# Optimization experiments

Measured on AMD Instinct MI355X. Metric: run time of the kernel, lower is better.

Reference implementation:

```python
import jax, jax.numpy as jnp
import numpy as np

# Problem constants (match init_kwargs)
T = 48            # prediction horizon
B = 1024          # batch size
A_SC = 0.999      # A_matrix[0,0]
B00, B01 = 0.95, -1.05   # B_matrix
SMIN, SMAX = 0.0, 13.5   # charge_min_max
PS_MAX = 5.0             # storage_power_min_max[1]
PG_MIN, PG_MAX = -10.0, 10.0  # grid_power_min_max
EPS_W = 1e4              # slack penalty weight in the objective
N_ITERS = 300            # PDHG iterations (fixed, jit-friendly)
DELTA = 1e-6             # tiny strong-convexity regularizer

# Variable layout in x (per sample): [s_0..s_T | Ps_in | Ps_out | Pl | Pr | eps]
# n = 6T+1. Equalities: dynamics (T rows) + s_0 == s0 (1 row). Inequalities: 12T rows.

def _build_matrices(T):
    n = 6 * T + 1
    off_in = T + 1; off_out = off_in + T; off_pl = off_out + T
    off_pr = off_pl + T; off_eps = off_pr + T
    # Equality block E x = b_eq
    E = np.zeros((T + 1, n), np.float32)
    idx = np.arange(T)
    E[idx, idx + 1] = 1.0          # s_{k+1}
    E[idx, idx] = -A_SC            # -A s_k
    E[idx, off_in + idx] = -B00    # -B00 Ps_in_k
    E[idx, off_out + idx] = -B01   # -B01 Ps_out_k
    E[T, 0] = 1.0                  # s_0 == s0
    I = np.eye(T, dtype=np.float32)
    def blk(*pairs):
        g = np.zeros((T, n), np.float32)
        for off, sgn in pairs:
            g[:, off:off + T] += sgn * I
        return g
    # Inequality block G x <= h, grouped by constraint type (order matches h below)
    G = np.concatenate([
        blk((0, -1.0)),                       # -s_k      <= -SMIN
        blk((0, 1.0)),                        #  s_k      <=  SMAX
        blk((off_in, 1.0)),                   #  Ps_in    <=  PS_MAX
        blk((off_in, -1.0)),                  # -Ps_in    <=  0
        blk((off_out, 1.0)),                  #  Ps_out   <=  PS_MAX
        blk((off_out, -1.0)),                 # -Ps_out   <=  0
        blk((off_pl, -1.0), (off_eps, -1.0)), # -Pl - eps <= -load
        blk((off_pl, 1.0), (off_eps, -1.0)),  #  Pl - eps <=  load
        blk((off_pr, -1.0), (off_eps, -1.0)), # -Pr - eps <= -pv
        blk((off_pr, 1.0), (off_eps, -1.0)),  #  Pr - eps <=  pv
        blk((off_pr, -1.0), (off_pl, 1.0), (off_in, 1.0), (off_out, -1.0)),  # -(grid) <= -PG_MIN
        blk((off_pr, 1.0), (off_pl, -1.0), (off_in, -1.0), (off_out, 1.0)),  #  (grid) <=  PG_MAX
    ], 0)
    K = np.concatenate([E, G], 0)
    knorm = float(np.linalg.norm(K, 2))
    return K, knorm

_K_NP, _KNORM = _build_matrices(T)
_K = jnp.asarray(_K_NP)  # (m, n), shared across the batch


def setup_inputs() -> dict:
    key = jax.random.key(0)
    k1, k2, k3, k4 = jax.random.split(key, 4)
    price = jax.random.uniform(k1, (B, T), jnp.float32) * 0.3 + 0.05  # $/kWh
    load = jax.random.uniform(k2, (B, T), jnp.float32) * 5.0           # kW
    pv = jax.random.uniform(k3, (B, T), jnp.float32) * 5.0             # kW
    s0 = jax.random.uniform(k4, (B, 1), jnp.float32) * 10.0 + 1.0      # kWh, in [SMIN,SMAX]
    return {"price_hat": price, "load_hat": load, "pv_hat": pv, "initial_state": s0}


def _solve(price, load, pv, s0):
    """Batched PDHG (Chambolle-Pock) solver for the per-sample LP.
    min c^T x + (DELTA/2)||x||^2  s.t.  E x = b_eq, G x <= h.
    """
    b = price.shape[0]
    zT = jnp.zeros((b, T), price.dtype)
    on = jnp.ones((b, T), price.dtype)
    # objective: -price*(Pr - Pl - Ps_in + Ps_out) + EPS_W*eps
    c = jnp.concatenate([jnp.zeros((b, T + 1), price.dtype),
                         price, -price, price, -price, EPS_W * on], 1)
    b_eq = jnp.concatenate([zT, s0], 1)  # dynamics rhs = 0, then s_0 = s0
    h = jnp.concatenate([-SMIN * on, SMAX * on, PS_MAX * on, zT, PS_MAX * on, zT,
                         -load, load, -pv, pv, -PG_MIN * on, PG_MAX * on], 1)
    q = jnp.concatenate([b_eq, h], 1)  # (b, m)
    n_eq = T + 1
    tau = 0.95 / _KNORM
    sigma = 0.95 / _KNORM
    n = c.shape[1]; m = q.shape[1]

    def step(carry, _):
        x, y = carry
        xn = (x - tau * (c + y @ _K)) / (1.0 + tau * DELTA)
        yb = y + sigma * ((2.0 * xn - x) @ _K.T) - sigma * q
        # equality duals are free; inequality duals projected to >= 0
        yn = jnp.concatenate([yb[:, :n_eq], jnp.maximum(yb[:, n_eq:], 0.0)], 1)
        return (xn, yn), None

    (x, _), _ = jax.lax.scan(step,
                             (jnp.zeros((b, n), price.dtype), jnp.zeros((b, m), price.dtype)),
                             None, length=N_ITERS)
    off = T + 1
    Ps_in = x[:, off:off + T]
    Ps_out = x[:, off + T:off + 2 * T]
    Pl = x[:, off + 2 * T:off + 3 * T]
    Pr = x[:, off + 3 * T:off + 4 * T]
    eps = x[:, off + 4 * T:off + 5 * T]
    return Ps_in, Ps_out, Pl, Pr, eps


def reference(price_hat, load_hat, pv_hat, initial_state):
    return _solve(price_hat, load_hat, pv_hat, initial_state)
```

## Files before the change

kernel.cpp:

```cpp
#include <hip/hip_runtime.h>
#include <math.h>


#define TT 48
#define N_ITERS 300

typedef float v2 __attribute__((ext_vector_type(2)));

__device__ __forceinline__ v2 vfma(v2 a, v2 b, v2 c) {
    return __builtin_elementwise_fma(a, b, c);
}
__device__ __forceinline__ v2 vmax0(v2 a) {
    return __builtin_elementwise_max(a, (v2)(0.f));
}

__device__ __forceinline__ float shift_up(float v, bool is0) {
    int iv  = __float_as_int(v);
    int s48 = __builtin_amdgcn_readlane(iv, 48);
    int sh  = __builtin_amdgcn_update_dpp(iv, iv, 0x138, 0xF, 0xF, false);
    sh = is0 ? s48 : sh;
    return __int_as_float(sh);
}

__device__ __forceinline__ float shift_dn(float v, bool is48) {
    int iv = __float_as_int(v);
    int s0 = __builtin_amdgcn_readlane(iv, 0);
    int sh = __builtin_amdgcn_update_dpp(iv, iv, 0x130, 0xF, 0xF, false);
    sh = is48 ? s0 : sh;
    return __int_as_float(sh);
}

__global__ __launch_bounds__(64) void pdhg_kernel(
    const float* __restrict__ price,
    const float* __restrict__ loadv,
    const float* __restrict__ pvv,
    const float* __restrict__ s0,
    float* __restrict__ out,
    int B,
    float tau)
{
    const int b = blockIdx.x;
    const int t = threadIdx.x;
    const bool lt  = (t < TT);
    const bool i48 = (t == 48);
    const bool i0  = (t == 0);

    const float A  = 0.999f;
    const float Bi = 0.95f;
    const float Bo = -1.05f;
    const float ts = tau * tau;

    float pr_ = 0.f, ld = 0.f, pv_ = 0.f;
    if (lt) {
        pr_ = price[(size_t)b*TT + t];
        ld  = loadv[(size_t)b*TT + t];
        pv_ = pvv  [(size_t)b*TT + t];
    }
    const float qe   = i48 ? s0[b] : 0.f;
    const float tsqe = ts * qe;

    const v2 tsv   = (v2)(ts);
    const v2 ntsv  = (v2)(-ts);
    const v2 npts  = { -ts, ts };
    const v2 BiBov = { -Bi, -Bo };
    const float tsA  = ts * A;
    const float tsBi = ts * Bi;
    const float tsBo = ts * Bo;
    const v2 tpv   = { tau * pr_, -tau * pr_ };
    const float tep = tau * 1.0e4f;
    const v2 C12   = { 0.f,        ts * 13.5f };
    const v2 C35   = { ts * 5.f,   ts * 5.f   };
    const v2 C79   = { ts * (-ld), ts * (-pv_) };
    const v2 C810  = { ts * ld,    ts * pv_   };
    const v2 C1112 = { ts * 10.f,  ts * 10.f  };

    v2 xIO = (v2)(0.f), xPP = (v2)(0.f), xSE = (v2)(0.f);
    float ye = 0.f, yprev = 0.f;
    v2 G12 = (v2)(0.f), G35 = (v2)(0.f), G46 = (v2)(0.f),
       G79 = (v2)(0.f), G810 = (v2)(0.f), G1112 = (v2)(0.f);

    #pragma unroll 2
    for (int it = 0; it < N_ITERS; ++it) {
        const v2 dv    = G1112 - G1112.yx;
        const v2 ktIO  = vfma((v2)(ye), BiBov, (G35 - G46) + dv);
        const v2 ktPP  = (G810 - G79) + dv;
        const v2 S     = G79 + G810;
        const float wep = tep - (S.x + S.y);
        float kts = fmaf(-A, ye, yprev + (G12.y - G12.x));
        kts = lt ? kts : yprev;

        const v2 wIO = ktIO + tpv;
        const v2 wPP = ktPP + tpv;
        const v2 wSE = { kts, wep };
        const v2 xnIO = xIO - wIO;  const v2 zIO = xnIO - wIO;
        const v2 xnPP = xPP - wPP;  const v2 zPP = xnPP - wPP;
        const v2 xnSE = xSE - wSE;  const v2 zSE = xnSE - wSE;
        const float zs = zSE.x;

        const float u0f = ye - tsqe;
        float uc = fmaf(-tsA,  zs,     u0f);
        uc       = fmaf(-tsBi, zIO.x,  uc);
        uc       = fmaf(-tsBo, zIO.y,  uc);
        const float u = lt ? uc : u0f;

        const float zsn = shift_dn(zs, i48);
        const float us  = shift_up(u,  i0);

        const v2 m11v = (zIO - zIO.yx) + (zPP - zPP.yx);
        G12   = vmax0(vfma(zSE.xx, npts, G12)  - C12);
        G35   = vmax0(vfma(zIO,    tsv,  G35)  - C35);
        G46   = vmax0(vfma(zIO,    ntsv, G46));
        G79   = vmax0(vfma(zSE.yy, ntsv, vfma(zPP, ntsv, G79))  - C79);
        G810  = vmax0(vfma(zSE.yy, ntsv, vfma(zPP, tsv,  G810)) - C810);
        G1112 = vmax0(vfma(m11v,   tsv,  G1112) - C1112);

        ye    = fmaf(ts, zsn, u);
        yprev = fmaf(ts, zs,  us);

        xSE = xnSE; xIO = xnIO; xPP = xnPP;
    }

    if (lt) {
        const size_t BT   = (size_t)B * TT;
        const size_t base = (size_t)b * TT + t;
        out[0*BT + base] = xIO.x;
        out[1*BT + base] = xIO.y;
        out[2*BT + base] = xPP.x;
        out[3*BT + base] = xPP.y;
        out[4*BT + base] = xSE.y;
    }
}

static float compute_tau_host()
{
    const double A = 0.999, Bi = 0.95, Bo = -1.05;
    const int n = 289;
    const int OS = 0, OI = 49, OO = 97, OPL = 145, OPR = 193, OE = 241;

    double q[289], qp[289], w[289];

    auto applyM = [&](const double* v, double* u) {
        double we[TT + 1];
        for (int t = 0; t < TT; ++t)
            we[t] = v[OS + t + 1] - A * v[OS + t] - Bi * v[OI + t] - Bo * v[OO + t];
        we[TT] = v[OS + 0];
        for (int j = 0; j <= TT; ++j) {
            double r = (j >= 1) ? we[j - 1] : we[TT];
            if (j <= TT - 1) r += -A * we[j] + 2.0 * v[OS + j];
            u[OS + j] = r;
        }
        for (int t = 0; t < TT; ++t) {
            const double w11 = v[OI + t] - v[OO + t] + v[OPL + t] - v[OPR + t];
            u[OI  + t] = -Bi * we[t] + 2.0 * v[OI  + t] + 2.0 * w11;
            u[OO  + t] = -Bo * we[t] + 2.0 * v[OO  + t] - 2.0 * w11;
            u[OPL + t] =  2.0 * v[OPL + t] + 2.0 * w11;
            u[OPR + t] =  2.0 * v[OPR + t] - 2.0 * w11;
            u[OE  + t] =  4.0 * v[OE  + t];
        }
    };

    unsigned long long lcg = 0x243F6A8885A308D3ull;
    for (int i = 0; i < n; ++i) {
        lcg = lcg * 6364136223846793005ull + 1442695040888963407ull;
        q[i] = ((double)(lcg >> 11) / 9007199254740992.0) - 0.5;
    }
    {
        double s = 0; for (int i = 0; i < n; ++i) s += q[i]*q[i];
        const double inv = 1.0 / sqrt(s);
        for (int i = 0; i < n; ++i) q[i] *= inv;
    }

    const int MMAX = 56;
    double alpha[MMAX], beta[MMAX];
    for (int i = 0; i < n; ++i) qp[i] = 0.0;
    double bprev = 0.0;
    int m = MMAX;
    for (int j = 0; j < MMAX; ++j) {
        applyM(q, w);
        if (j > 0) for (int i = 0; i < n; ++i) w[i] -= bprev * qp[i];
        double a = 0; for (int i = 0; i < n; ++i) a += w[i] * q[i];
        alpha[j] = a;
        for (int i = 0; i < n; ++i) w[i] -= a * q[i];
        double s = 0; for (int i = 0; i < n; ++i) s += w[i]*w[i];
        const double bnx = sqrt(s);
        if (bnx < 1e-12) { m = j + 1; break; }
        beta[j] = bnx;
        const double inv = 1.0 / bnx;
        for (int i = 0; i < n; ++i) { qp[i] = q[i]; q[i] = w[i] * inv; }
        bprev = bnx;
    }

    double hi = 0.0;
    for (int i = 0; i < m; ++i) {
        double g = alpha[i] + (i > 0 ? fabs(beta[i-1]) : 0.0)
                            + (i < m-1 ? fabs(beta[i]) : 0.0);
        if (g > hi) hi = g;
    }
    hi += 1e-9; double lo = 0.0;
    for (int it = 0; it < 64; ++it) {
        const double mid = 0.5 * (lo + hi);
        int cnt = 0; double d = 1.0;
        for (int i = 0; i < m; ++i) {
            double tt = alpha[i] - mid - (i > 0 ? beta[i-1]*beta[i-1] / d : 0.0);
            if (tt < 0) ++cnt;
            if (fabs(tt) < 1e-30) tt = -1e-30;
            d = tt;
        }
        if (cnt >= m) hi = mid; else lo = mid;
    }
    double lam = 0.5 * (lo + hi);

    applyM(q, w);
    double rq = 0, nq = 0;
    for (int i = 0; i < n; ++i) { rq += q[i]*w[i]; nq += q[i]*q[i]; }
    rq /= nq;
    if (rq > lam) lam = rq;

    return (float)(0.95 / sqrt(lam));
}

extern "C" void kernel_launch(void* const* d_in, const int* in_sizes, int n_in,
                              void* d_out, int out_size, void* d_ws, size_t ws_size,
                              hipStream_t stream)
{
    const float* price = (const float*)d_in[0];
    const float* loadv = (const float*)d_in[1];
    const float* pvv   = (const float*)d_in[2];
    const float* s0    = (const float*)d_in[3];
    float* out = (float*)d_out;

    const int B = in_sizes[0] / TT;
    const float tau = compute_tau_host();

    pdhg_kernel<<<B, 64, 0, stream>>>(price, loadv, pvv, s0, out, B, tau);
}
```

Before: 43.79 us.

## Pack eight samples per block and use shuffles for lane shifts

Launches 8 waves per block, one sample per wave, instead of one 64-thread block per sample. The DPP plus readlane lane shifts become __shfl with precomputed neighbour lanes. Lane-dependent selects are folded into per-lane constants so the loop has fewer conditionals. __shfl on AMD lowers to ds_bpermute through LDS hardware, which adds latency to the serial 300-iteration dependency chain. It also cuts block count from 1024 to 128, which may under-fill the GPU's CUs.

After: 67.33 us. +53.8%, slower.

```diff
diff --git a/kernel.cpp b/kernel.cpp
--- a/kernel.cpp
+++ b/kernel.cpp
@@ -4,6 +4,7 @@
 
 #define TT 48
 #define N_ITERS 300
+#define WPB 8
 
 typedef float v2 __attribute__((ext_vector_type(2)));
 
@@ -14,23 +15,7 @@
     return __builtin_elementwise_max(a, (v2)(0.f));
 }
 
-__device__ __forceinline__ float shift_up(float v, bool is0) {
-    int iv  = __float_as_int(v);
-    int s48 = __builtin_amdgcn_readlane(iv, 48);
-    int sh  = __builtin_amdgcn_update_dpp(iv, iv, 0x138, 0xF, 0xF, false);
-    sh = is0 ? s48 : sh;
-    return __int_as_float(sh);
-}
-
-__device__ __forceinline__ float shift_dn(float v, bool is48) {
-    int iv = __float_as_int(v);
-    int s0 = __builtin_amdgcn_readlane(iv, 0);
-    int sh = __builtin_amdgcn_update_dpp(iv, iv, 0x130, 0xF, 0xF, false);
-    sh = is48 ? s0 : sh;
-    return __int_as_float(sh);
-}
-
-__global__ __launch_bounds__(64) void pdhg_kernel(
+__global__ __launch_bounds__(WPB * 64) void pdhg_kernel(
     const float* __restrict__ price,
     const float* __restrict__ loadv,
     const float* __restrict__ pvv,
@@ -39,11 +24,13 @@
     int B,
     float tau)
 {
-    const int b = blockIdx.x;
-    const int t = threadIdx.x;
+    const int wave = threadIdx.x >> 6;
+    const int t    = threadIdx.x & 63;
+    const int b    = blockIdx.x * WPB + wave;
+    if (b >= B) return;
+
     const bool lt  = (t < TT);
-    const bool i48 = (t == 48);
-    const bool i0  = (t == 0);
+    const bool i48 = (t == TT);
 
     const float A  = 0.999f;
     const float Bi = 0.95f;
@@ -61,18 +48,22 @@
 
     const v2 tsv   = (v2)(ts);
     const v2 ntsv  = (v2)(-ts);
-    const v2 npts  = { -ts, ts };
+    const v2 npts  = lt ? (v2){ -ts, ts } : (v2){ 0.f, 0.f };
     const v2 BiBov = { -Bi, -Bo };
-    const float tsA  = ts * A;
-    const float tsBi = ts * Bi;
-    const float tsBo = ts * Bo;
+    const float Avec  = lt ? A       : 0.f;
+    const float tsAl  = lt ? ts * A  : 0.f;
+    const float tsBil = lt ? ts * Bi : 0.f;
+    const float tsBol = lt ? ts * Bo : 0.f;
     const v2 tpv   = { tau * pr_, -tau * pr_ };
     const float tep = tau * 1.0e4f;
-    const v2 C12   = { 0.f,        ts * 13.5f };
+    const v2 C12   = lt ? (v2){ 0.f, ts * 13.5f } : (v2){ 0.f, 0.f };
     const v2 C35   = { ts * 5.f,   ts * 5.f   };
     const v2 C79   = { ts * (-ld), ts * (-pv_) };
     const v2 C810  = { ts * ld,    ts * pv_   };
     const v2 C1112 = { ts * 10.f,  ts * 10.f  };
+
+    const int prevLane = (t == 0)  ? TT : (t - 1);
+    const int nextLane = (t >= TT) ? 0  : (t + 1);
 
     v2 xIO = (v2)(0.f), xPP = (v2)(0.f), xSE = (v2)(0.f);
     float ye = 0.f, yprev = 0.f;
@@ -86,8 +77,7 @@
         const v2 ktPP  = (G810 - G79) + dv;
         const v2 S     = G79 + G810;
         const float wep = tep - (S.x + S.y);
-        float kts = fmaf(-A, ye, yprev + (G12.y - G12.x));
-        kts = lt ? kts : yprev;
+        const float kts = fmaf(-Avec, ye, yprev + (G12.y - G12.x));
 
         const v2 wIO = ktIO + tpv;
         const v2 wPP = ktPP + tpv;
@@ -97,14 +87,13 @@
         const v2 xnSE = xSE - wSE;  const v2 zSE = xnSE - wSE;
         const float zs = zSE.x;
 
-        const float u0f = ye - tsqe;
-        float uc = fmaf(-tsA,  zs,     u0f);
-        uc       = fmaf(-tsBi, zIO.x,  uc);
-        uc       = fmaf(-tsBo, zIO.y,  uc);
-        const float u = lt ? uc : u0f;
-
-        const float zsn = shift_dn(zs, i48);
-        const float us  = shift_up(u,  i0);
+        float u = ye - tsqe;
+        u = fmaf(-tsBol, zIO.y, u);
+        u = fmaf(-tsBil, zIO.x, u);
+        u = fmaf(-tsAl,  zs,    u);
+
+        const float zsn = __shfl(zs, nextLane);
+        const float us  = __shfl(u,  prevLane);
 
         const v2 m11v = (zIO - zIO.yx) + (zPP - zPP.yx);
         G12   = vmax0(vfma(zSE.xx, npts, G12)  - C12);
@@ -232,5 +221,6 @@
     const int B = in_sizes[0] / TT;
     const float tau = compute_tau_host();
 
-    pdhg_kernel<<<B, 64, 0, stream>>>(price, loadv, pvv, s0, out, B, tau);
-}
+    const int grid = (B + WPB - 1) / WPB;
+    pdhg_kernel<<<grid, WPB * 64, 0, stream>>>(price, loadv, pvv, s0, out, B, tau);
+}
```
